# Optimization experiments

Measured on AMD Instinct MI355X. Metric: run time of the kernel, lower is better.

The kernel has to match this reference:

```python
import jax, jax.numpy as jnp
import numpy as np

N_LOCAL = 400
N_VOXEL = 200_000
N_EDGES = 1_200_000
D_LOCAL = 19
D_VOXEL = 6
NUM_CLASSES = 7
HIDDEN = 128
EPS = 1e-5  # GraphNorm eps


def _graph_norm(x, w, b, ms):
    # PyG GraphNorm with a single graph (batch=None): subtract scaled mean,
    # normalize by mean of squared centered values.
    mean = jnp.mean(x, axis=0, keepdims=True)
    out = x - ms * mean
    var = jnp.mean(out * out, axis=0, keepdims=True)
    return w * out * jax.lax.rsqrt(var + EPS) + b


def _gcn(x, src, dst, dinv, W, b, n):
    # GCNConv: symmetric-normalized aggregation with self-loops (already in src/dst)
    xw = x @ W
    msg = xw[src] * (dinv[src] * dinv[dst])[:, None]
    return jax.ops.segment_sum(msg, dst, num_segments=n) + b


def setup_inputs() -> dict:
    key = jax.random.key(0)
    ks = jax.random.split(key, 32)

    def p(k, shape, fan):
        return (jax.random.normal(k, shape, jnp.float32) / np.float32(np.sqrt(fan)))

    inp = {}
    inp["local_x"] = jax.random.normal(ks[0], (N_LOCAL, D_LOCAL), jnp.float32)
    inp["local_type"] = jax.random.randint(ks[1], (N_LOCAL,), 0, NUM_CLASSES)
    inp["voxel_x"] = jax.random.normal(ks[2], (N_VOXEL, D_VOXEL), jnp.float32)
    inp["voxel_type"] = jax.random.randint(ks[3], (N_VOXEL,), 0, NUM_CLASSES)
    inp["edge_index"] = jax.random.randint(ks[4], (2, N_EDGES), 0, N_VOXEL)
    inp["label_hard"] = jax.random.uniform(ks[5], (1, N_VOXEL, NUM_CLASSES), jnp.float32)

    din = D_LOCAL + D_VOXEL + NUM_CLASSES  # 32
    inp["We1"] = p(ks[6], (din, HIDDEN), din); inp["be1"] = jnp.zeros((HIDDEN,), jnp.float32)
    inp["We2"] = p(ks[7], (HIDDEN, HIDDEN), HIDDEN); inp["be2"] = jnp.zeros((HIDDEN,), jnp.float32)

    # encoder conv channels: 128->64->32->64->128 (REPEAT=2 down, then 2 up)
    conv_dims = [(128, 64), (64, 32), (32, 64), (64, 128)]
    for i, (a, b_) in enumerate(conv_dims):
        inp[f"Wc{i}"] = p(ks[8 + i], (a, b_), a)
        inp[f"bc{i}"] = jnp.zeros((b_,), jnp.float32)
        inp[f"gw{i}"] = jnp.ones((b_,), jnp.float32)
        inp[f"gb{i}"] = jnp.zeros((b_,), jnp.float32)
        inp[f"gm{i}"] = jnp.ones((b_,), jnp.float32)

    dec_dims = [(128, 64), (64, 32), (32, 16), (16, 1)]
    for i, (a, b_) in enumerate(dec_dims):
        inp[f"Wd{i}"] = p(ks[16 + i], (a, b_), a)
        inp[f"bd{i}"] = jnp.zeros((b_,), jnp.float32)
    return inp


def reference(local_x, local_type, voxel_x, voxel_type, edge_index, label_hard,
              We1, be1, We2, be2,
              Wc0, bc0, gw0, gb0, gm0,
              Wc1, bc1, gw1, gb1, gm1,
              Wc2, bc2, gw2, gb2, gm2,
              Wc3, bc3, gw3, gb3, gm3,
              Wd0, bd0, Wd1, bd1, Wd2, bd2, Wd3, bd3):
    n = voxel_x.shape[0]

    # --- masked type-match mean aggregation (vectorized segment mean) ---
    ones = jnp.ones((local_x.shape[0],), local_x.dtype)
    cnt = jax.ops.segment_sum(ones, local_type, num_segments=NUM_CLASSES)
    sums = jax.ops.segment_sum(local_x, local_type, num_segments=NUM_CLASSES)
    means = jnp.where(cnt[:, None] > 0, sums / jnp.maximum(cnt, 1.0)[:, None], 0.0)
    matched = means[voxel_type]  # [N_v, D_LOCAL]; zeros where type absent locally

    x = jnp.concatenate([matched, voxel_x, label_hard[0]], axis=-1)
    x = jax.nn.relu(x @ We1 + be1)
    x = jax.nn.relu(x @ We2 + be2)

    # --- GCN normalization with self-loops, computed once ---
    loop = jnp.arange(n)
    src = jnp.concatenate([edge_index[0], loop])
    dst = jnp.concatenate([edge_index[1], loop])
    deg = jax.ops.segment_sum(jnp.ones_like(dst, dtype=x.dtype), dst, num_segments=n)
    dinv = jax.lax.rsqrt(jnp.maximum(deg, 1.0))

    layers = [(Wc0, bc0, gw0, gb0, gm0), (Wc1, bc1, gw1, gb1, gm1),
              (Wc2, bc2, gw2, gb2, gm2), (Wc3, bc3, gw3, gb3, gm3)]
    for (W, b, gw, gb, gm) in layers:  # conv -> GraphNorm -> ReLU (Dropout = eval identity)
        x = _gcn(x, src, dst, dinv, W, b, n)
        x = jax.nn.relu(_graph_norm(x, gw, gb, gm))

    x = jax.nn.relu(x @ Wd0 + bd0)
    x = jax.nn.relu(x @ Wd1 + bd1)
    x = jax.nn.relu(x @ Wd2 + bd2)
    return jax.nn.sigmoid(x @ Wd3 + bd3)  # [N_v, 1]
```

## Files before the change

### kernel.cpp

```cpp
#include <hip/hip_runtime.h>
#include <hip/hip_bf16.h>
#include <cstddef>

#define THREADS 256
#define NSLOT 64

typedef unsigned short ushort_t;
typedef unsigned int uint_t;

__device__ __forceinline__ float b2f(ushort_t u) {
    union { float f; uint_t i; } v; v.i = ((uint_t)u) << 16; return v.f;
}
__device__ __forceinline__ ushort_t f2b(float f) {
    uint_t i = __float_as_uint(f);
    uint_t r = i + 0x7fffu + ((i >> 16) & 1u);
    return (ushort_t)(r >> 16);
}
__device__ __forceinline__ void unpack8(uint4 r, float* v) {
    v[0] = b2f(r.x & 0xffff); v[1] = b2f(r.x >> 16);
    v[2] = b2f(r.y & 0xffff); v[3] = b2f(r.y >> 16);
    v[4] = b2f(r.z & 0xffff); v[5] = b2f(r.z >> 16);
    v[6] = b2f(r.w & 0xffff); v[7] = b2f(r.w >> 16);
}
__device__ __forceinline__ uint4 pack8(const float* v) {
    uint4 r;
    r.x = (uint_t)f2b(v[0]) | ((uint_t)f2b(v[1]) << 16);
    r.y = (uint_t)f2b(v[2]) | ((uint_t)f2b(v[3]) << 16);
    r.z = (uint_t)f2b(v[4]) | ((uint_t)f2b(v[5]) << 16);
    r.w = (uint_t)f2b(v[6]) | ((uint_t)f2b(v[7]) << 16);
    return r;
}


__global__ __launch_bounds__(256) void local_means_kernel(const float* __restrict__ lx,
                                                          const int* __restrict__ lt,
                                                          float* __restrict__ means, int nl)
{
    __shared__ float slx[512 * 19];
    __shared__ int   slt[512];
    const int tid = threadIdx.x;
    for (int i = tid; i < nl * 19; i += 256) slx[i] = lx[i];
    for (int i = tid; i < nl; i += 256) slt[i] = lt[i];
    __syncthreads();
    if (tid >= 7 * 19) return;
    int c = tid / 19, dd = tid % 19;
    float s = 0.f; int cnt = 0;
    for (int i = 0; i < nl; ++i) {
        if (slt[i] == c) { s += slx[i * 19 + dd]; cnt++; }
    }
    means[tid] = cnt > 0 ? s / (float)cnt : 0.f;
}

__global__ void hist_kernel(const int* __restrict__ dst, int* __restrict__ degi, int E)
{
    int t = blockIdx.x * THREADS + threadIdx.x;
    if (t < E) atomicAdd(&degi[dst[t]], 1);
}


__global__ __launch_bounds__(256) void scan_part1_kernel(const int* __restrict__ degi,
                                                         int* __restrict__ blocksums, int n)
{
    const int tid = threadIdx.x;
    const int idx = blockIdx.x * 1024 + tid * 4;
    int v = 0;
    if (idx + 3 < n) {
        int4 d = *(const int4*)&degi[idx];
        v = d.x + d.y + d.z + d.w;
    } else {
        for (int i = 0; i < 4; ++i) if (idx + i < n) v += degi[idx + i];
    }
    __shared__ int s[256];
    s[tid] = v;
    __syncthreads();
    for (int off = 128; off >= 1; off >>= 1) {
        if (tid < off) s[tid] += s[tid + off];
        __syncthreads();
    }
    if (tid == 0) blocksums[blockIdx.x] = s[0];
}

__global__ __launch_bounds__(256) void scan_part2_kernel(int* __restrict__ blocksums, int nb)
{
    __shared__ int s[256];
    const int tid = threadIdx.x;
    int v = (tid < nb) ? blocksums[tid] : 0;
    s[tid] = v;
    __syncthreads();
    for (int off = 1; off < 256; off <<= 1) {
        int t = (tid >= off) ? s[tid - off] : 0;
        __syncthreads();
        s[tid] += t;
        __syncthreads();
    }
    if (tid < nb) blocksums[tid] = s[tid] - v;
}

__global__ __launch_bounds__(256) void scan_part3_kernel(const int* __restrict__ degi,
                                                         const int* __restrict__ blocksums,
                                                         int* __restrict__ rowptr,
                                                         int* __restrict__ cursor,
                                                         float* __restrict__ dinv, int n, int E)
{
    const int tid = threadIdx.x;
    const int idx = blockIdx.x * 1024 + tid * 4;
    int d0 = 0, d1 = 0, d2 = 0, d3 = 0;
    if (idx + 3 < n) {
        int4 d = *(const int4*)&degi[idx];
        d0 = d.x; d1 = d.y; d2 = d.z; d3 = d.w;
    } else {
        if (idx     < n) d0 = degi[idx];
        if (idx + 1 < n) d1 = degi[idx + 1];
        if (idx + 2 < n) d2 = degi[idx + 2];
        if (idx + 3 < n) d3 = degi[idx + 3];
    }
    const int v = d0 + d1 + d2 + d3;
    __shared__ int s[256];
    s[tid] = v;
    __syncthreads();
    for (int off = 1; off < 256; off <<= 1) {
        int t = (tid >= off) ? s[tid - off] : 0;
        __syncthreads();
        s[tid] += t;
        __syncthreads();
    }
    int run = blocksums[blockIdx.x] + s[tid] - v;
    if (idx + 3 < n) {
        int4 o;
        o.x = run; run += d0;
        o.y = run; run += d1;
        o.z = run; run += d2;
        o.w = run;
        *(int4*)&rowptr[idx] = o;
        *(int4*)&cursor[idx] = o;
        float4 dv;
        dv.x = rsqrtf((float)d0 + 1.0f);
        dv.y = rsqrtf((float)d1 + 1.0f);
        dv.z = rsqrtf((float)d2 + 1.0f);
        dv.w = rsqrtf((float)d3 + 1.0f);
        *(float4*)&dinv[idx] = dv;
    } else {
        if (idx     < n) { rowptr[idx]     = run; cursor[idx]     = run; dinv[idx]     = rsqrtf((float)d0 + 1.0f); run += d0; }
        if (idx + 1 < n) { rowptr[idx + 1] = run; cursor[idx + 1] = run; dinv[idx + 1] = rsqrtf((float)d1 + 1.0f); run += d1; }
        if (idx + 2 < n) { rowptr[idx + 2] = run; cursor[idx + 2] = run; dinv[idx + 2] = rsqrtf((float)d2 + 1.0f); run += d2; }
        if (idx + 3 < n) { rowptr[idx + 3] = run; cursor[idx + 3] = run; dinv[idx + 3] = rsqrtf((float)d3 + 1.0f); }
    }
    if (blockIdx.x == 0 && tid == 0) rowptr[n] = E;
}

__global__ void fill_kernel(const int* __restrict__ src, const int* __restrict__ dst,
                            int* __restrict__ cursor, int* __restrict__ esrc, int E)
{
    int t = blockIdx.x * THREADS + threadIdx.x;
    if (t >= E) return;
    int s = src[t], d = dst[t];
    int pos = atomicAdd(&cursor[d], 1);
    esrc[pos] = s;
}

__global__ void build_x0_kernel(const float* __restrict__ means,
                                const int* __restrict__ vt,
                                const float* __restrict__ vx,
                                const float* __restrict__ label,
                                float* __restrict__ out, int n)
{
    int tid = blockIdx.x * THREADS + threadIdx.x;
    int node = tid >> 5, c = tid & 31;
    if (node >= n) return;
    float v;
    if (c < 19)      v = means[vt[node] * 19 + c];
    else if (c < 25) v = vx[node * 6 + (c - 19)];
    else             v = label[node * 7 + (c - 25)];
    out[(size_t)node * 32 + c] = v;
}

template<int D>
__global__ void transform_kernel(const float* __restrict__ x, ushort_t* __restrict__ out,
                                 const float* __restrict__ tr, const float* __restrict__ dinv, int n)
{
    constexpr int Q = D / 8;
    int t = blockIdx.x * THREADS + threadIdx.x;
    int node = t / Q, q = t % Q;
    if (node >= n) return;
    float v[8], o[8];
    *(float4*)&v[0] = *(const float4*)&x[(size_t)node * D + q * 8];
    *(float4*)&v[4] = *(const float4*)&x[(size_t)node * D + q * 8 + 4];
    const float dd = dinv[node];
#pragma unroll
    for (int e = 0; e < 8; ++e) {
        o[e] = fmaxf(fmaf(v[e], tr[q * 8 + e], tr[D + q * 8 + e]), 0.f) * dd;
    }
    *(uint4*)&out[(size_t)node * D + q * 8] = pack8(o);
}

template<int DIN, int DOUT, int BN, int JPER, bool RELU, bool BIAS, bool TRANSFORM, bool SCALE, bool OUTBF>
__global__ __launch_bounds__(256) void mlp_kernel(
    const float* __restrict__ in, void* __restrict__ out_v,
    const float* __restrict__ W, const float* __restrict__ bias,
    const float* __restrict__ tr ,
    const float* __restrict__ rowscale, int n)
{
    constexpr int KT  = 32;
    constexpr int TJ  = DOUT / JPER;
    constexpr int TN  = 256 / TJ;
    constexpr int NPT = BN / TN;
    constexpr int JQ  = JPER / 4;
    constexpr int CS  = 4 * TJ;
    constexpr int BNP = BN + 4;

    __shared__ float Wt[KT * DOUT];
    __shared__ float xT[KT][BNP];

    const int tid   = threadIdx.x;
    const int nbase = blockIdx.x * BN;
    const int tj = tid % TJ, tn = tid / TJ;
    const int j0 = tj * 4, n0 = tn * NPT;

    float acc[NPT][JPER];
#pragma unroll
    for (int p = 0; p < NPT; ++p)
#pragma unroll
        for (int j = 0; j < JPER; ++j) acc[p][j] = 0.f;

    for (int kt = 0; kt < DIN; kt += KT) {
        __syncthreads();
        for (int i = tid * 4; i < KT * DOUT; i += THREADS * 4) {
            *(float4*)&Wt[i] = *(const float4*)&W[(size_t)kt * DOUT + i];
        }
        for (int i = tid; i < BN * (KT / 4); i += THREADS) {
            int node = i / (KT / 4);
            int kq   = i % (KT / 4);
            int g    = nbase + node;
            float4 v = make_float4(0.f, 0.f, 0.f, 0.f);
            if (g < n) {
                v = *(const float4*)&in[(size_t)g * DIN + kt + kq * 4];
                if (TRANSFORM) {
                    const float4 a = *(const float4*)&tr[kt + kq * 4];
                    const float4 c = *(const float4*)&tr[DIN + kt + kq * 4];
                    v.x = fmaxf(fmaf(v.x, a.x, c.x), 0.f);
                    v.y = fmaxf(fmaf(v.y, a.y, c.y), 0.f);
                    v.z = fmaxf(fmaf(v.z, a.z, c.z), 0.f);
                    v.w = fmaxf(fmaf(v.w, a.w, c.w), 0.f);
                }
            }
            xT[kq * 4 + 0][node] = v.x;
            xT[kq * 4 + 1][node] = v.y;
            xT[kq * 4 + 2][node] = v.z;
            xT[kq * 4 + 3][node] = v.w;
        }
        __syncthreads();
#pragma unroll 4
        for (int kk = 0; kk < KT; ++kk) {
            float wv[JPER];
#pragma unroll
            for (int q = 0; q < JQ; ++q)
                *(float4*)&wv[q * 4] = *(const float4*)&Wt[kk * DOUT + q * CS + j0];
            float xv[NPT];
#pragma unroll
            for (int q = 0; q < NPT / 4; ++q)
                *(float4*)&xv[q * 4] = *(const float4*)&xT[kk][n0 + q * 4];
#pragma unroll
            for (int p = 0; p < NPT; ++p)
#pragma unroll
                for (int j = 0; j < JPER; ++j)
                    acc[p][j] = fmaf(xv[p], wv[j], acc[p][j]);
        }
    }

    float bv[JPER];
#pragma unroll
    for (int j = 0; j < JPER; ++j) bv[j] = 0.f;
    if (BIAS) {
#pragma unroll
        for (int q = 0; q < JQ; ++q)
            *(float4*)&bv[q * 4] = *(const float4*)&bias[q * CS + j0];
    }

#pragma unroll
    for (int p = 0; p < NPT; ++p) {
        const int g = nbase + n0 + p;
        if (g >= n) continue;
        float rs = 1.f;
        if (SCALE) rs = rowscale[g];
#pragma unroll
        for (int q = 0; q < JQ; ++q) {
            float o[4];
#pragma unroll
            for (int e = 0; e < 4; ++e) {
                float x = acc[p][q * 4 + e] + bv[q * 4 + e];
                if (RELU) x = fmaxf(x, 0.f);
                if (SCALE) x *= rs;
                o[e] = x;
            }
            if (OUTBF) {
                ushort4 ob;
                ob.x = f2b(o[0]); ob.y = f2b(o[1]); ob.z = f2b(o[2]); ob.w = f2b(o[3]);
                *(ushort4*)&((ushort_t*)out_v)[(size_t)g * DOUT + q * CS + j0] = ob;
            } else {
                *(float4*)&((float*)out_v)[(size_t)g * DOUT + q * CS + j0] =
                    make_float4(o[0], o[1], o[2], o[3]);
            }
        }
    }
}

template<int D>
__global__ __launch_bounds__(256) void gather_agg_kernel(
    const ushort_t* __restrict__ y, float* __restrict__ out,
    const int* __restrict__ rowptr, const int* __restrict__ esrc,
    const float* __restrict__ dinv,
    const float* __restrict__ bias, float* __restrict__ statsP, int n)
{
    constexpr int JT  = D / 8;
    constexpr int NPB = 256 / JT;
    const int tid  = threadIdx.x;
    const int jq   = tid % JT;
    const int nsub = tid / JT;
    const int j0   = jq * 8;

    float bv[8];
#pragma unroll
    for (int e = 0; e < 8; ++e) bv[e] = bias[j0 + e];

    float s1[8], s2[8];
#pragma unroll
    for (int e = 0; e < 8; ++e) { s1[e] = 0.f; s2[e] = 0.f; }

    const int ntiles = (n + NPB - 1) / NPB;
    for (int tile = blockIdx.x; tile < ntiles; tile += gridDim.x) {
        const int node = tile * NPB + nsub;
        if (node < n) {
            const int rb = rowptr[node], re = rowptr[node + 1];
            const float dd = dinv[node];
            float acc[8];
            unpack8(*(const uint4*)&y[(size_t)node * D + j0], acc);
            int k = rb;
            for (; k + 3 < re; k += 4) {
                const int sa = esrc[k], sb = esrc[k + 1];
                const int sc = esrc[k + 2], sd = esrc[k + 3];
                const uint4 r0 = *(const uint4*)&y[(size_t)sa * D + j0];
                const uint4 r1 = *(const uint4*)&y[(size_t)sb * D + j0];
                const uint4 r2 = *(const uint4*)&y[(size_t)sc * D + j0];
                const uint4 r3 = *(const uint4*)&y[(size_t)sd * D + j0];
                float v0[8], v1[8], v2[8], v3[8];
                unpack8(r0, v0); unpack8(r1, v1); unpack8(r2, v2); unpack8(r3, v3);
#pragma unroll
                for (int e = 0; e < 8; ++e) acc[e] += (v0[e] + v1[e]) + (v2[e] + v3[e]);
            }
            for (; k < re; ++k) {
                float va[8];
                unpack8(*(const uint4*)&y[(size_t)esrc[k] * D + j0], va);
#pragma unroll
                for (int e = 0; e < 8; ++e) acc[e] += va[e];
            }
            float o[8];
#pragma unroll
            for (int e = 0; e < 8; ++e) {
                o[e] = fmaf(acc[e], dd, bv[e]);
                s1[e] += o[e];
                s2[e] = fmaf(o[e], o[e], s2[e]);
            }
            *(float4*)&out[(size_t)node * D + j0]     = make_float4(o[0], o[1], o[2], o[3]);
            *(float4*)&out[(size_t)node * D + j0 + 4] = make_float4(o[4], o[5], o[6], o[7]);
        }
    }

    __shared__ float red[256][17];
#pragma unroll
    for (int e = 0; e < 8; ++e) { red[tid][e] = s1[e]; red[tid][8 + e] = s2[e]; }
    __syncthreads();
#pragma unroll
    for (int off = NPB / 2; off >= 1; off >>= 1) {
        if (nsub < off) {
#pragma unroll
            for (int e = 0; e < 16; ++e) red[tid][e] += red[tid + off * JT][e];
        }
        __syncthreads();
    }
    if (nsub == 0) {
        float* slot = statsP + (size_t)(blockIdx.x & (NSLOT - 1)) * 256;
#pragma unroll
        for (int e = 0; e < 8; ++e) {
            atomicAdd(&slot[j0 + e],     red[tid][e]);
            atomicAdd(&slot[D + j0 + e], red[tid][8 + e]);
        }
    }
}

template<int D>
__global__ __launch_bounds__(256) void gather_pre_kernel(
    const ushort_t* __restrict__ x, float* __restrict__ out,
    const int* __restrict__ rowptr, const int* __restrict__ esrc,
    const float* __restrict__ dinv, int n)
{
    constexpr int JT  = D / 8;
    constexpr int NPB = 256 / JT;
    const int tid  = threadIdx.x;
    const int jq   = tid % JT;
    const int nsub = tid / JT;
    const int j0   = jq * 8;

    const int ntiles = (n + NPB - 1) / NPB;
    for (int tile = blockIdx.x; tile < ntiles; tile += gridDim.x) {
        const int node = tile * NPB + nsub;
        if (node < n) {
            const int rb = rowptr[node], re = rowptr[node + 1];
            const float dd = dinv[node];
            float acc[8];
            unpack8(*(const uint4*)&x[(size_t)node * D + j0], acc);
            int k = rb;
            for (; k + 3 < re; k += 4) {
                const int sa = esrc[k], sb = esrc[k + 1];
                const int sc = esrc[k + 2], sd = esrc[k + 3];
                const uint4 r0 = *(const uint4*)&x[(size_t)sa * D + j0];
                const uint4 r1 = *(const uint4*)&x[(size_t)sb * D + j0];
                const uint4 r2 = *(const uint4*)&x[(size_t)sc * D + j0];
                const uint4 r3 = *(const uint4*)&x[(size_t)sd * D + j0];
                float v0[8], v1[8], v2[8], v3[8];
                unpack8(r0, v0); unpack8(r1, v1); unpack8(r2, v2); unpack8(r3, v3);
#pragma unroll
                for (int e = 0; e < 8; ++e) acc[e] += (v0[e] + v1[e]) + (v2[e] + v3[e]);
            }
            for (; k < re; ++k) {
                float va[8];
                unpack8(*(const uint4*)&x[(size_t)esrc[k] * D + j0], va);
#pragma unroll
                for (int e = 0; e < 8; ++e) acc[e] += va[e];
            }
            float o[8];
#pragma unroll
            for (int e = 0; e < 8; ++e) o[e] = acc[e] * dd;
            *(float4*)&out[(size_t)node * D + j0]     = make_float4(o[0], o[1], o[2], o[3]);
            *(float4*)&out[(size_t)node * D + j0 + 4] = make_float4(o[4], o[5], o[6], o[7]);
        }
    }
}

template<int D>
__global__ __launch_bounds__(256) void gn_stats_kernel(const float* __restrict__ x,
                                                       float* __restrict__ statsP, int n)
{
    constexpr int JT   = D / 4;
    constexpr int NPB  = 256 / JT;
    constexpr int ITER = 32;
    const int tid  = threadIdx.x;
    const int jb   = tid % JT;
    const int rsub = tid / JT;
    const int j0   = jb * 4;
    const int base = blockIdx.x * NPB * ITER;

    float s1[4] = {0.f, 0.f, 0.f, 0.f};
    float s2[4] = {0.f, 0.f, 0.f, 0.f};

#pragma unroll 4
    for (int i = 0; i < ITER; ++i) {
        int r = base + rsub + i * NPB;
        if (r < n) {
            float4 v = *(const float4*)&x[(size_t)r * D + j0];
            s1[0] += v.x; s1[1] += v.y; s1[2] += v.z; s1[3] += v.w;
            s2[0] = fmaf(v.x, v.x, s2[0]);
            s2[1] = fmaf(v.y, v.y, s2[1]);
            s2[2] = fmaf(v.z, v.z, s2[2]);
            s2[3] = fmaf(v.w, v.w, s2[3]);
        }
    }

    __shared__ float red[256][9];
#pragma unroll
    for (int e = 0; e < 4; ++e) { red[tid][e] = s1[e]; red[tid][4 + e] = s2[e]; }
    __syncthreads();
#pragma unroll
    for (int off = NPB / 2; off >= 1; off >>= 1) {
        if (rsub < off) {
#pragma unroll
            for (int e = 0; e < 8; ++e) red[tid][e] += red[tid + off * JT][e];
        }
        __syncthreads();
    }
    if (rsub == 0) {
        float* slot = statsP + (size_t)(blockIdx.x & (NSLOT - 1)) * 256;
#pragma unroll
        for (int e = 0; e < 4; ++e) {
            atomicAdd(&slot[j0 + e],     red[tid][e]);
            atomicAdd(&slot[D + j0 + e], red[tid][4 + e]);
        }
    }
}

template<int D>
__global__ void gn_finalize_kernel(const float* __restrict__ part, float* __restrict__ ac,
                                   const float* __restrict__ gw, const float* __restrict__ gb,
                                   const float* __restrict__ gm, float inv_n)
{
    int j = threadIdx.x;
    if (j >= D) return;
    float s1 = 0.f, s2 = 0.f;
    for (int t = 0; t < NSLOT; ++t) {
        s1 += part[(size_t)t * 256 + j];
        s2 += part[(size_t)t * 256 + D + j];
    }
    float mean = s1 * inv_n;
    float ex2  = s2 * inv_n;
    float m    = gm[j];
    float var  = ex2 - (2.f * m - m * m) * mean * mean;
    float a    = gw[j] * rsqrtf(var + 1e-5f);
    float c    = gb[j] - a * m * mean;
    ac[j]     = a;
    ac[D + j] = c;
}

__global__ __launch_bounds__(256) void dec_tail_kernel(
    const float* __restrict__ in, const float* __restrict__ W1, const float* __restrict__ b1,
    const float* __restrict__ W2, const float* __restrict__ b2,
    const float* __restrict__ W3, const float* __restrict__ b3,
    float* __restrict__ out, int n)
{
    int t = blockIdx.x * THREADS + threadIdx.x;
    if (t >= n) return;

    float x[64];
#pragma unroll
    for (int q = 0; q < 16; ++q)
        *(float4*)&x[q * 4] = *(const float4*)&in[(size_t)t * 64 + q * 4];

    float h1[32];
#pragma unroll
    for (int j = 0; j < 32; ++j) h1[j] = b1[j];
#pragma unroll 8
    for (int k = 0; k < 64; ++k) {
        const float xk = x[k];
#pragma unroll
        for (int j = 0; j < 32; ++j) h1[j] = fmaf(xk, W1[k * 32 + j], h1[j]);
    }
#pragma unroll
    for (int j = 0; j < 32; ++j) h1[j] = fmaxf(h1[j], 0.f);

    float h2[16];
#pragma unroll
    for (int j = 0; j < 16; ++j) h2[j] = b2[j];
#pragma unroll 8
    for (int k = 0; k < 32; ++k) {
        const float hk = h1[k];
#pragma unroll
        for (int j = 0; j < 16; ++j) h2[j] = fmaf(hk, W2[k * 16 + j], h2[j]);
    }

    float acc = b3[0];
#pragma unroll
    for (int k = 0; k < 16; ++k) acc = fmaf(fmaxf(h2[k], 0.f), W3[k], acc);
    out[t] = 1.0f / (1.0f + expf(-acc));
}


extern "C" void kernel_launch(void* const* d_in, const int* in_sizes, int n_in,
                              void* d_out, int out_size, void* d_ws, size_t ws_size,
                              hipStream_t stream)
{
    const float* local_x    = (const float*)d_in[0];
    const int*   local_type = (const int*)d_in[1];
    const float* voxel_x    = (const float*)d_in[2];
    const int*   voxel_type = (const int*)d_in[3];
    const int*   edge_index = (const int*)d_in[4];
    const float* label      = (const float*)d_in[5];
    const float* We1 = (const float*)d_in[6],  *be1 = (const float*)d_in[7];
    const float* We2 = (const float*)d_in[8],  *be2 = (const float*)d_in[9];
    const float *Wc[4], *bc[4], *gw[4], *gb[4], *gm[4];
    for (int i = 0; i < 4; ++i) {
        Wc[i] = (const float*)d_in[10 + i * 5];
        bc[i] = (const float*)d_in[11 + i * 5];
        gw[i] = (const float*)d_in[12 + i * 5];
        gb[i] = (const float*)d_in[13 + i * 5];
        gm[i] = (const float*)d_in[14 + i * 5];
    }
    const float* Wd0 = (const float*)d_in[30], *bd0 = (const float*)d_in[31];
    const float* Wd1 = (const float*)d_in[32], *bd1 = (const float*)d_in[33];
    const float* Wd2 = (const float*)d_in[34], *bd2 = (const float*)d_in[35];
    const float* Wd3 = (const float*)d_in[36], *bd3 = (const float*)d_in[37];

    const int n  = in_sizes[2] / 6;
    const int E  = in_sizes[4] / 2;
    const int nl = in_sizes[0] / 19;
    const int* src = edge_index;
    const int* dst = edge_index + E;

    auto align256 = [](size_t x) { return (x + 255) & ~(size_t)255; };
    char* w = (char*)d_ws;
    float* ac_all = (float*)w;
    float* means  = (float*)(w + 4096);
    int* blocksums = (int*)(w + 8192);
    float* stats_part = (float*)(w + 8192 + 1024);
    size_t off = 8192 + 1024 + 4 * NSLOT * 256 * sizeof(float);
    int*   rowptr = (int*)(w + off);   off += align256((size_t)(n + 1) * 4);
    float* dinv   = (float*)(w + off); off += align256((size_t)n * 4);
    int*   esrc   = (int*)(w + off);   off += align256((size_t)E * 4);
    float* A  = (float*)(w + off);
    float* B  = A + (size_t)n * 128;
    ushort_t* Y = (ushort_t*)(B + (size_t)n * 128);
    float* A2 = A + (size_t)n * 64;
    float* B2 = B + (size_t)n * 64;
    int*   degi   = (int*)A;
    int*   cursor = (int*)A2;

    const float inv_n = 1.0f / (float)n;
    auto cdiv = [](long long a, long long b) { return (int)((a + b - 1) / b); };
    const int nb = cdiv(n, 1024);

    float* part0 = stats_part + 0 * NSLOT * 256;
    float* part1 = stats_part + 1 * NSLOT * 256;
    float* part2 = stats_part + 2 * NSLOT * 256;
    float* part3 = stats_part + 3 * NSLOT * 256;
    float* ac0 = ac_all + 0, *ac1 = ac_all + 256, *ac2 = ac_all + 512, *ac3 = ac_all + 768;

    hipMemsetAsync(stats_part, 0, 4 * NSLOT * 256 * sizeof(float), stream);
    hipMemsetAsync(degi, 0, (size_t)n * sizeof(int), stream);

    local_means_kernel<<<1, 256, 0, stream>>>(local_x, local_type, means, nl);
    hist_kernel<<<cdiv(E, 256), 256, 0, stream>>>(dst, degi, E);
    scan_part1_kernel<<<nb, 256, 0, stream>>>(degi, blocksums, n);
    scan_part2_kernel<<<1, 256, 0, stream>>>(blocksums, nb);
    scan_part3_kernel<<<nb, 256, 0, stream>>>(degi, blocksums, rowptr, cursor, dinv, n, E);
    fill_kernel<<<cdiv(E, 256), 256, 0, stream>>>(src, dst, cursor, esrc, E);
    build_x0_kernel<<<cdiv((long long)n * 32, 256), 256, 0, stream>>>(means, voxel_type, voxel_x, label, B, n);

    const int gagg = 2048;

    mlp_kernel<32, 128, 128, 8, true, true, false, false, false><<<cdiv(n, 128), 256, 0, stream>>>(B, A, We1, be1, nullptr, nullptr, n);
    mlp_kernel<128, 128, 128, 8, true, true, false, false, false><<<cdiv(n, 128), 256, 0, stream>>>(A, B, We2, be2, nullptr, nullptr, n);

    mlp_kernel<128, 64, 256, 8, false, false, false, true, true><<<cdiv(n, 256), 256, 0, stream>>>(B, Y, Wc[0], nullptr, nullptr, dinv, n);
    gather_agg_kernel<64><<<gagg, 256, 0, stream>>>(Y, A2, rowptr, esrc, dinv, bc[0], part0, n);
    gn_finalize_kernel<64><<<1, 64, 0, stream>>>(part0, ac0, gw[0], gb[0], gm[0], inv_n);

    mlp_kernel<64, 32, 256, 4, false, false, true, true, true><<<cdiv(n, 256), 256, 0, stream>>>(A2, Y, Wc[1], nullptr, ac0, dinv, n);
    gather_agg_kernel<32><<<gagg, 256, 0, stream>>>(Y, B2, rowptr, esrc, dinv, bc[1], part1, n);
    gn_finalize_kernel<32><<<1, 32, 0, stream>>>(part1, ac1, gw[1], gb[1], gm[1], inv_n);

    transform_kernel<32><<<cdiv((long long)n * 4, 256), 256, 0, stream>>>(B2, Y, ac1, dinv, n);
    gather_pre_kernel<32><<<gagg, 256, 0, stream>>>(Y, A, rowptr, esrc, dinv, n);
    mlp_kernel<32, 64, 256, 8, false, true, false, false, false><<<cdiv(n, 256), 256, 0, stream>>>(A, A2, Wc[2], bc[2], nullptr, nullptr, n);
    gn_stats_kernel<64><<<cdiv(n, 512), 256, 0, stream>>>(A2, part2, n);
    gn_finalize_kernel<64><<<1, 64, 0, stream>>>(part2, ac2, gw[2], gb[2], gm[2], inv_n);

    transform_kernel<64><<<cdiv((long long)n * 8, 256), 256, 0, stream>>>(A2, Y, ac2, dinv, n);
    gather_pre_kernel<64><<<gagg, 256, 0, stream>>>(Y, B, rowptr, esrc, dinv, n);
    mlp_kernel<64, 128, 128, 8, false, true, false, false, false><<<cdiv(n, 128), 256, 0, stream>>>(B, A, Wc[3], bc[3], nullptr, nullptr, n);
    gn_stats_kernel<128><<<cdiv(n, 256), 256, 0, stream>>>(A, part3, n);
    gn_finalize_kernel<128><<<1, 128, 0, stream>>>(part3, ac3, gw[3], gb[3], gm[3], inv_n);

    mlp_kernel<128, 64, 256, 8, true, true, true, false, false><<<cdiv(n, 256), 256, 0, stream>>>(A, B, Wd0, bd0, ac3, nullptr, n);
    dec_tail_kernel<<<cdiv(n, 256), 256, 0, stream>>>(B, Wd1, bd1, Wd2, bd2, Wd3, bd3, (float*)d_out, n);
}
```

Measured before the change: 812.1 us.

## Use bf16 MFMA for large MLP layers and switch gather buffers to fp32

Adds an MFMA-based matmul kernel that converts activations and weights to bf16 in shared memory and uses 16x16x32 bf16 matrix instructions for the 128-wide layers. It replaces the FMA tiled kernel for the second encoder layer, the first conv, the last conv and the first decoder layer. At the same time the intermediate gather buffers go from bf16 to fp32, which removes pack/unpack work but doubles bytes moved in the edge gathers. The MFMA epilogue writes scalar per-column stores, which may coalesce less well.

```diff
diff --git a/kernel.cpp b/kernel.cpp
--- a/kernel.cpp
+++ b/kernel.cpp
@@ -7,28 +7,13 @@
 
 typedef unsigned short ushort_t;
 typedef unsigned int uint_t;
-
-__device__ __forceinline__ float b2f(ushort_t u) {
-    union { float f; uint_t i; } v; v.i = ((uint_t)u) << 16; return v.f;
-}
+typedef __attribute__((ext_vector_type(8))) short bf16x8;
+typedef __attribute__((ext_vector_type(4))) float f32x4;
+
 __device__ __forceinline__ ushort_t f2b(float f) {
     uint_t i = __float_as_uint(f);
     uint_t r = i + 0x7fffu + ((i >> 16) & 1u);
     return (ushort_t)(r >> 16);
-}
-__device__ __forceinline__ void unpack8(uint4 r, float* v) {
-    v[0] = b2f(r.x & 0xffff); v[1] = b2f(r.x >> 16);
-    v[2] = b2f(r.y & 0xffff); v[3] = b2f(r.y >> 16);
-    v[4] = b2f(r.z & 0xffff); v[5] = b2f(r.z >> 16);
-    v[6] = b2f(r.w & 0xffff); v[7] = b2f(r.w >> 16);
-}
-__device__ __forceinline__ uint4 pack8(const float* v) {
-    uint4 r;
-    r.x = (uint_t)f2b(v[0]) | ((uint_t)f2b(v[1]) << 16);
-    r.y = (uint_t)f2b(v[2]) | ((uint_t)f2b(v[3]) << 16);
-    r.z = (uint_t)f2b(v[4]) | ((uint_t)f2b(v[5]) << 16);
-    r.w = (uint_t)f2b(v[6]) | ((uint_t)f2b(v[7]) << 16);
-    return r;
 }
 
 
@@ -56,7 +41,6 @@
     int t = blockIdx.x * THREADS + threadIdx.x;
     if (t < E) atomicAdd(&degi[dst[t]], 1);
 }
-
 
 __global__ __launch_bounds__(256) void scan_part1_kernel(const int* __restrict__ degi,
                                                          int* __restrict__ blocksums, int n)
@@ -175,30 +159,30 @@
 }
 
 template<int D>
-__global__ void transform_kernel(const float* __restrict__ x, ushort_t* __restrict__ out,
+__global__ void transform_kernel(const float* __restrict__ x, float* __restrict__ out,
                                  const float* __restrict__ tr, const float* __restrict__ dinv, int n)
 {
-    constexpr int Q = D / 8;
+    constexpr int Q = D / 4;
     int t = blockIdx.x * THREADS + threadIdx.x;
     int node = t / Q, q = t % Q;
     if (node >= n) return;
-    float v[8], o[8];
-    *(float4*)&v[0] = *(const float4*)&x[(size_t)node * D + q * 8];
-    *(float4*)&v[4] = *(const float4*)&x[(size_t)node * D + q * 8 + 4];
+    float4 v = *(const float4*)&x[(size_t)node * D + q * 4];
+    const float4 a = *(const float4*)&tr[q * 4];
+    const float4 c = *(const float4*)&tr[D + q * 4];
     const float dd = dinv[node];
-#pragma unroll
-    for (int e = 0; e < 8; ++e) {
-        o[e] = fmaxf(fmaf(v[e], tr[q * 8 + e], tr[D + q * 8 + e]), 0.f) * dd;
-    }
-    *(uint4*)&out[(size_t)node * D + q * 8] = pack8(o);
-}
-
-template<int DIN, int DOUT, int BN, int JPER, bool RELU, bool BIAS, bool TRANSFORM, bool SCALE, bool OUTBF>
+    float4 o;
+    o.x = fmaxf(fmaf(v.x, a.x, c.x), 0.f) * dd;
+    o.y = fmaxf(fmaf(v.y, a.y, c.y), 0.f) * dd;
+    o.z = fmaxf(fmaf(v.z, a.z, c.z), 0.f) * dd;
+    o.w = fmaxf(fmaf(v.w, a.w, c.w), 0.f) * dd;
+    *(float4*)&out[(size_t)node * D + q * 4] = o;
+}
+
+template<int DIN, int DOUT, int BN, int JPER, bool RELU, bool BIAS, bool TRANSFORM, bool SCALE>
 __global__ __launch_bounds__(256) void mlp_kernel(
-    const float* __restrict__ in, void* __restrict__ out_v,
+    const float* __restrict__ in, float* __restrict__ out,
     const float* __restrict__ W, const float* __restrict__ bias,
-    const float* __restrict__ tr ,
-    const float* __restrict__ rowscale, int n)
+    const float* __restrict__ tr, const float* __restrict__ rowscale, int n)
 {
     constexpr int KT  = 32;
     constexpr int TJ  = DOUT / JPER;
@@ -284,21 +268,126 @@
         if (SCALE) rs = rowscale[g];
 #pragma unroll
         for (int q = 0; q < JQ; ++q) {
-            float o[4];
-#pragma unroll
-            for (int e = 0; e < 4; ++e) {
-                float x = acc[p][q * 4 + e] + bv[q * 4 + e];
-                if (RELU) x = fmaxf(x, 0.f);
-                if (SCALE) x *= rs;
-                o[e] = x;
-            }
-            if (OUTBF) {
-                ushort4 ob;
-                ob.x = f2b(o[0]); ob.y = f2b(o[1]); ob.z = f2b(o[2]); ob.w = f2b(o[3]);
-                *(ushort4*)&((ushort_t*)out_v)[(size_t)g * DOUT + q * CS + j0] = ob;
-            } else {
-                *(float4*)&((float*)out_v)[(size_t)g * DOUT + q * CS + j0] =
-                    make_float4(o[0], o[1], o[2], o[3]);
+            float4 o;
+            o.x = acc[p][q * 4 + 0] + bv[q * 4 + 0];
+            o.y = acc[p][q * 4 + 1] + bv[q * 4 + 1];
+            o.z = acc[p][q * 4 + 2] + bv[q * 4 + 2];
+            o.w = acc[p][q * 4 + 3] + bv[q * 4 + 3];
+            if (RELU) {
+                o.x = fmaxf(o.x, 0.f); o.y = fmaxf(o.y, 0.f);
+                o.z = fmaxf(o.z, 0.f); o.w = fmaxf(o.w, 0.f);
+            }
+            if (SCALE) { o.x *= rs; o.y *= rs; o.z *= rs; o.w *= rs; }
+            *(float4*)&out[(size_t)g * DOUT + q * CS + j0] = o;
+        }
+    }
+}
+
+template<int DIN, int DOUT, bool RELU, bool BIAS, bool TRANSFORM, bool SCALE>
+__global__ __launch_bounds__(256) void mfma_mlp_kernel(
+    const float* __restrict__ in, float* __restrict__ out,
+    const float* __restrict__ W, const float* __restrict__ bias,
+    const float* __restrict__ tr, const float* __restrict__ rowscale, int n)
+{
+    constexpr int BN  = 128;
+    constexpr int KT  = 32;
+    constexpr int NT  = DIN / KT;
+    constexpr int LDK = 40;
+    constexpr int WM  = 2, WN = 2;
+    constexpr int MW  = BN / WM;
+    constexpr int NW  = DOUT / WN;
+    constexpr int MR  = MW / 16;
+    constexpr int NR  = NW / 16;
+
+    __shared__ ushort_t xA[BN * LDK];
+    __shared__ ushort_t wB[DOUT * LDK];
+
+    const int tid   = threadIdx.x;
+    const int wid   = tid >> 6;
+    const int lane  = tid & 63;
+    const int wm    = wid >> 1, wn = wid & 1;
+    const int nbase = blockIdx.x * BN;
+    const int l16   = lane & 15;
+    const int lk8   = (lane >> 4) * 8;
+
+    f32x4 acc[MR][NR];
+#pragma unroll
+    for (int mi = 0; mi < MR; ++mi)
+#pragma unroll
+        for (int ni = 0; ni < NR; ++ni)
+#pragma unroll
+            for (int j = 0; j < 4; ++j) acc[mi][ni][j] = 0.f;
+
+    for (int t = 0; t < NT; ++t) {
+        const int kt = t * KT;
+        __syncthreads();
+        for (int i = tid; i < BN * (KT / 4); i += 256) {
+            const int row = i / (KT / 4);
+            const int kq  = (i % (KT / 4)) * 4;
+            const int g   = nbase + row;
+            float4 v = make_float4(0.f, 0.f, 0.f, 0.f);
+            if (g < n) {
+                v = *(const float4*)&in[(size_t)g * DIN + kt + kq];
+                if (TRANSFORM) {
+                    const float4 a = *(const float4*)&tr[kt + kq];
+                    const float4 c = *(const float4*)&tr[DIN + kt + kq];
+                    v.x = fmaxf(fmaf(v.x, a.x, c.x), 0.f);
+                    v.y = fmaxf(fmaf(v.y, a.y, c.y), 0.f);
+                    v.z = fmaxf(fmaf(v.z, a.z, c.z), 0.f);
+                    v.w = fmaxf(fmaf(v.w, a.w, c.w), 0.f);
+                }
+            }
+            ushort4 b;
+            b.x = f2b(v.x); b.y = f2b(v.y); b.z = f2b(v.z); b.w = f2b(v.w);
+            *(ushort4*)&xA[row * LDK + kq] = b;
+        }
+        for (int i = tid; i < (KT * DOUT) / 4; i += 256) {
+            const int k = (i * 4) / DOUT;
+            const int c = (i * 4) % DOUT;
+            float4 v = *(const float4*)&W[(size_t)(kt + k) * DOUT + c];
+            wB[(c + 0) * LDK + k] = f2b(v.x);
+            wB[(c + 1) * LDK + k] = f2b(v.y);
+            wB[(c + 2) * LDK + k] = f2b(v.z);
+            wB[(c + 3) * LDK + k] = f2b(v.w);
+        }
+        __syncthreads();
+
+        bf16x8 af[MR], bf[NR];
+#pragma unroll
+        for (int mi = 0; mi < MR; ++mi)
+            af[mi] = *(const bf16x8*)&xA[(wm * MW + mi * 16 + l16) * LDK + lk8];
+#pragma unroll
+        for (int ni = 0; ni < NR; ++ni)
+            bf[ni] = *(const bf16x8*)&wB[(wn * NW + ni * 16 + l16) * LDK + lk8];
+#pragma unroll
+        for (int mi = 0; mi < MR; ++mi)
+#pragma unroll
+            for (int ni = 0; ni < NR; ++ni)
+                acc[mi][ni] = __builtin_amdgcn_mfma_f32_16x16x32_bf16(
+                    af[mi], bf[ni], acc[mi][ni], 0, 0, 0);
+    }
+
+    float bv[NR];
+#pragma unroll
+    for (int ni = 0; ni < NR; ++ni)
+        bv[ni] = BIAS ? bias[wn * NW + ni * 16 + l16] : 0.f;
+
+#pragma unroll
+    for (int mi = 0; mi < MR; ++mi) {
+#pragma unroll
+        for (int j = 0; j < 4; ++j) {
+            const int r = wm * MW + mi * 16 + (lane >> 4) * 4 + j;
+            const int g = nbase + r;
+            if (g >= n) continue;
+            float rs = 1.f;
+            if (SCALE) rs = rowscale[g];
+#pragma unroll
+            for (int ni = 0; ni < NR; ++ni) {
+                const int col = wn * NW + ni * 16 + l16;
+                float v = acc[mi][ni][j] + bv[ni];
+                if (RELU) v = fmaxf(v, 0.f);
+                if (SCALE) v *= rs;
+                out[(size_t)g * DOUT + col] = v;
             }
         }
     }
@@ -306,7 +395,7 @@
 
 template<int D>
 __global__ __launch_bounds__(256) void gather_agg_kernel(
-    const ushort_t* __restrict__ y, float* __restrict__ out,
+    const float* __restrict__ y, float* __restrict__ out,
     const int* __restrict__ rowptr, const int* __restrict__ esrc,
     const float* __restrict__ dinv,
     const float* __restrict__ bias, float* __restrict__ statsP, int n)
@@ -333,25 +422,26 @@
             const int rb = rowptr[node], re = rowptr[node + 1];
             const float dd = dinv[node];
             float acc[8];
-            unpack8(*(const uint4*)&y[(size_t)node * D + j0], acc);
+            *(float4*)&acc[0] = *(const float4*)&y[(size_t)node * D + j0];
+            *(float4*)&acc[4] = *(const float4*)&y[(size_t)node * D + j0 + 4];
             int k = rb;
-            for (; k + 3 < re; k += 4) {
+            for (; k + 1 < re; k += 2) {
                 const int sa = esrc[k], sb = esrc[k + 1];
-                const int sc = esrc[k + 2], sd = esrc[k + 3];
-                const uint4 r0 = *(const uint4*)&y[(size_t)sa * D + j0];
-                const uint4 r1 = *(const uint4*)&y[(size_t)sb * D + j0];
-                const uint4 r2 = *(const uint4*)&y[(size_t)sc * D + j0];
-                const uint4 r3 = *(const uint4*)&y[(size_t)sd * D + j0];
-                float v0[8], v1[8], v2[8], v3[8];
-                unpack8(r0, v0); unpack8(r1, v1); unpack8(r2, v2); unpack8(r3, v3);
-#pragma unroll
-                for (int e = 0; e < 8; ++e) acc[e] += (v0[e] + v1[e]) + (v2[e] + v3[e]);
-            }
-            for (; k < re; ++k) {
-                float va[8];
-                unpack8(*(const uint4*)&y[(size_t)esrc[k] * D + j0], va);
-#pragma unroll
-                for (int e = 0; e < 8; ++e) acc[e] += va[e];
+                float4 a0 = *(const float4*)&y[(size_t)sa * D + j0];
+                float4 a1 = *(const float4*)&y[(size_t)sa * D + j0 + 4];
+                float4 b0 = *(const float4*)&y[(size_t)sb * D + j0];
+                float4 b1 = *(const float4*)&y[(size_t)sb * D + j0 + 4];
+                acc[0] += a0.x + b0.x; acc[1] += a0.y + b0.y;
+                acc[2] += a0.z + b0.z; acc[3] += a0.w + b0.w;
+                acc[4] += a1.x + b1.x; acc[5] += a1.y + b1.y;
+                acc[6] += a1.z + b1.z; acc[7] += a1.w + b1.w;
+            }
+            if (k < re) {
+                const int sa = esrc[k];
+                float4 a0 = *(const float4*)&y[(size_t)sa * D + j0];
+                float4 a1 = *(const float4*)&y[(size_t)sa * D + j0 + 4];
+                acc[0] += a0.x; acc[1] += a0.y; acc[2] += a0.z; acc[3] += a0.w;
+                acc[4] += a1.x; acc[5] += a1.y; acc[6] += a1.z; acc[7] += a1.w;
             }
             float o[8];
 #pragma unroll
@@ -389,7 +479,7 @@
 
 template<int D>
 __global__ __launch_bounds__(256) void gather_pre_kernel(
-    const ushort_t* __restrict__ x, float* __restrict__ out,
+    const float* __restrict__ x, float* __restrict__ out,
     const int* __restrict__ rowptr, const int* __restrict__ esrc,
     const float* __restrict__ dinv, int n)
 {
@@ -407,31 +497,31 @@
             const int rb = rowptr[node], re = rowptr[node + 1];
             const float dd = dinv[node];
             float acc[8];
-            unpack8(*(const uint4*)&x[(size_t)node * D + j0], acc);
+            *(float4*)&acc[0] = *(const float4*)&x[(size_t)node * D + j0];
+            *(float4*)&acc[4] = *(const float4*)&x[(size_t)node * D + j0 + 4];
             int k = rb;
-            for (; k + 3 < re; k += 4) {
+            for (; k + 1 < re; k += 2) {
                 const int sa = esrc[k], sb = esrc[k + 1];
-                const int sc = esrc[k + 2], sd = esrc[k + 3];
-                const uint4 r0 = *(const uint4*)&x[(size_t)sa * D + j0];
-                const uint4 r1 = *(const uint4*)&x[(size_t)sb * D + j0];
-                const uint4 r2 = *(const uint4*)&x[(size_t)sc * D + j0];
-                const uint4 r3 = *(const uint4*)&x[(size_t)sd * D + j0];
-                float v0[8], v1[8], v2[8], v3[8];
-                unpack8(r0, v0); unpack8(r1, v1); unpack8(r2, v2); unpack8(r3, v3);
-#pragma unroll
-                for (int e = 0; e < 8; ++e) acc[e] += (v0[e] + v1[e]) + (v2[e] + v3[e]);
-            }
-            for (; k < re; ++k) {
-                float va[8];
-                unpack8(*(const uint4*)&x[(size_t)esrc[k] * D + j0], va);
-#pragma unroll
-                for (int e = 0; e < 8; ++e) acc[e] += va[e];
-            }
-            float o[8];
-#pragma unroll
-            for (int e = 0; e < 8; ++e) o[e] = acc[e] * dd;
-            *(float4*)&out[(size_t)node * D + j0]     = make_float4(o[0], o[1], o[2], o[3]);
-            *(float4*)&out[(size_t)node * D + j0 + 4] = make_float4(o[4], o[5], o[6], o[7]);
+                float4 a0 = *(const float4*)&x[(size_t)sa * D + j0];
+                float4 a1 = *(const float4*)&x[(size_t)sa * D + j0 + 4];
+                float4 b0 = *(const float4*)&x[(size_t)sb * D + j0];
+                float4 b1 = *(const float4*)&x[(size_t)sb * D + j0 + 4];
+                acc[0] += a0.x + b0.x; acc[1] += a0.y + b0.y;
+                acc[2] += a0.z + b0.z; acc[3] += a0.w + b0.w;
+                acc[4] += a1.x + b1.x; acc[5] += a1.y + b1.y;
+                acc[6] += a1.z + b1.z; acc[7] += a1.w + b1.w;
+            }
+            if (k < re) {
+                const int sa = esrc[k];
+                float4 a0 = *(const float4*)&x[(size_t)sa * D + j0];
+                float4 a1 = *(const float4*)&x[(size_t)sa * D + j0 + 4];
+                acc[0] += a0.x; acc[1] += a0.y; acc[2] += a0.z; acc[3] += a0.w;
+                acc[4] += a1.x; acc[5] += a1.y; acc[6] += a1.z; acc[7] += a1.w;
+            }
+            float4 o0 = make_float4(acc[0] * dd, acc[1] * dd, acc[2] * dd, acc[3] * dd);
+            float4 o1 = make_float4(acc[4] * dd, acc[5] * dd, acc[6] * dd, acc[7] * dd);
+            *(float4*)&out[(size_t)node * D + j0]     = o0;
+            *(float4*)&out[(size_t)node * D + j0 + 4] = o1;
         }
     }
 }
@@ -593,13 +683,14 @@
     int*   rowptr = (int*)(w + off);   off += align256((size_t)(n + 1) * 4);
     float* dinv   = (float*)(w + off); off += align256((size_t)n * 4);
     int*   esrc   = (int*)(w + off);   off += align256((size_t)E * 4);
-    float* A  = (float*)(w + off);
-    float* B  = A + (size_t)n * 128;
-    ushort_t* Y = (ushort_t*)(B + (size_t)n * 128);
-    float* A2 = A + (size_t)n * 64;
-    float* B2 = B + (size_t)n * 64;
+    float* A    = (float*)(w + off);
+    float* B    = A + (size_t)n * 128;
+    float* A_lo = A;
+    float* A_hi = A + (size_t)n * 64;
+    float* B_lo = B;
+    float* B_hi = B + (size_t)n * 64;
     int*   degi   = (int*)A;
-    int*   cursor = (int*)A2;
+    int*   cursor = (int*)A_hi;
 
     const float inv_n = 1.0f / (float)n;
     auto cdiv = [](long long a, long long b) { return (int)((a + b - 1) / b); };
@@ -620,33 +711,34 @@
     scan_part2_kernel<<<1, 256, 0, stream>>>(blocksums, nb);
     scan_part3_kernel<<<nb, 256, 0, stream>>>(degi, blocksums, rowptr, cursor, dinv, n, E);
     fill_kernel<<<cdiv(E, 256), 256, 0, stream>>>(src, dst, cursor, esrc, E);
-    build_x0_kernel<<<cdiv((long long)n * 32, 256), 256, 0, stream>>>(means, voxel_type, voxel_x, label, B, n);
-
-    const int gagg = 2048;
-
-    mlp_kernel<32, 128, 128, 8, true, true, false, false, false><<<cdiv(n, 128), 256, 0, stream>>>(B, A, We1, be1, nullptr, nullptr, n);
-    mlp_kernel<128, 128, 128, 8, true, true, false, false, false><<<cdiv(n, 128), 256, 0, stream>>>(A, B, We2, be2, nullptr, nullptr, n);
-
-    mlp_kernel<128, 64, 256, 8, false, false, false, true, true><<<cdiv(n, 256), 256, 0, stream>>>(B, Y, Wc[0], nullptr, nullptr, dinv, n);
-    gather_agg_kernel<64><<<gagg, 256, 0, stream>>>(Y, A2, rowptr, esrc, dinv, bc[0], part0, n);
+    build_x0_kernel<<<cdiv((long long)n * 32, 256), 256, 0, stream>>>(means, voxel_type, voxel_x, label, B_lo, n);
+
+    const int gagg  = 2048;
+    const int gmfma = cdiv(n, 128);
+
+    mlp_kernel<32, 128, 128, 8, true, true, false, false><<<cdiv(n, 128), 256, 0, stream>>>(B_lo, A, We1, be1, nullptr, nullptr, n);
+    mfma_mlp_kernel<128, 128, true, true, false, false><<<gmfma, 256, 0, stream>>>(A, B, We2, be2, nullptr, nullptr, n);
+
+    mfma_mlp_kernel<128, 64, false, false, false, true><<<gmfma, 256, 0, stream>>>(B, A_lo, Wc[0], nullptr, nullptr, dinv, n);
+    gather_agg_kernel<64><<<gagg, 256, 0, stream>>>(A_lo, A_hi, rowptr, esrc, dinv, bc[0], part0, n);
     gn_finalize_kernel<64><<<1, 64, 0, stream>>>(part0, ac0, gw[0], gb[0], gm[0], inv_n);
 
-    mlp_kernel<64, 32, 256, 4, false, false, true, true, true><<<cdiv(n, 256), 256, 0, stream>>>(A2, Y, Wc[1], nullptr, ac0, dinv, n);
-    gather_agg_kernel<32><<<gagg, 256, 0, stream>>>(Y, B2, rowptr, esrc, dinv, bc[1], part1, n);
+    mlp_kernel<64, 32, 256, 4, false, false, true, true><<<cdiv(n, 256), 256, 0, stream>>>(A_hi, B_lo, Wc[1], nullptr, ac0, dinv, n);
+    gather_agg_kernel<32><<<gagg, 256, 0, stream>>>(B_lo, B_hi, rowptr, esrc, dinv, bc[1], part1, n);
     gn_finalize_kernel<32><<<1, 32, 0, stream>>>(part1, ac1, gw[1], gb[1], gm[1], inv_n);
 
-    transform_kernel<32><<<cdiv((long long)n * 4, 256), 256, 0, stream>>>(B2, Y, ac1, dinv, n);
-    gather_pre_kernel<32><<<gagg, 256, 0, stream>>>(Y, A, rowptr, esrc, dinv, n);
-    mlp_kernel<32, 64, 256, 8, false, true, false, false, false><<<cdiv(n, 256), 256, 0, stream>>>(A, A2, Wc[2], bc[2], nullptr, nullptr, n);
-    gn_stats_kernel<64><<<cdiv(n, 512), 256, 0, stream>>>(A2, part2, n);
+    transform_kernel<32><<<cdiv((long long)n * 8, 256), 256, 0, stream>>>(B_hi, B_lo, ac1, dinv, n);
+    gather_pre_kernel<32><<<gagg, 256, 0, stream>>>(B_lo, A_lo, rowptr, esrc, dinv, n);
+    mlp_kernel<32, 64, 256, 8, false, true, false, false><<<cdiv(n, 256), 256, 0, stream>>>(A_lo, B_hi, Wc[2], bc[2], nullptr, nullptr, n);
+    gn_stats_kernel<64><<<cdiv(n, 512), 256, 0, stream>>>(B_hi, part2, n);
     gn_finalize_kernel<64><<<1, 64, 0, stream>>>(part2, ac2, gw[2], gb[2], gm[2], inv_n);
 
-    transform_kernel<64><<<cdiv((long long)n * 8, 256), 256, 0, stream>>>(A2, Y, ac2, dinv, n);
-    gather_pre_kernel<64><<<gagg, 256, 0, stream>>>(Y, B, rowptr, esrc, dinv, n);
-    mlp_kernel<64, 128, 128, 8, false, true, false, false, false><<<cdiv(n, 128), 256, 0, stream>>>(B, A, Wc[3], bc[3], nullptr, nullptr, n);
+    transform_kernel<64><<<cdiv((long long)n * 16, 256), 256, 0, stream>>>(B_hi, A_lo, ac2, dinv, n);
+    gather_pre_kernel<64><<<gagg, 256, 0, stream>>>(A_lo, B_lo, rowptr, esrc, dinv, n);
+    mfma_mlp_kernel<64, 128, false, true, false, false><<<gmfma, 256, 0, stream>>>(B_lo, A, Wc[3], bc[3], nullptr, nullptr, n);
     gn_stats_kernel<128><<<cdiv(n, 256), 256, 0, stream>>>(A, part3, n);
     gn_finalize_kernel<128><<<1, 128, 0, stream>>>(part3, ac3, gw[3], gb[3], gm[3], inv_n);
 
-    mlp_kernel<128, 64, 256, 8, true, true, true, false, false><<<cdiv(n, 256), 256, 0, stream>>>(A, B, Wd0, bd0, ac3, nullptr, n);
-    dec_tail_kernel<<<cdiv(n, 256), 256, 0, stream>>>(B, Wd1, bd1, Wd2, bd2, Wd3, bd3, (float*)d_out, n);
-}
+    mfma_mlp_kernel<128, 64, true, true, true, false><<<gmfma, 256, 0, stream>>>(A, B_lo, Wd0, bd0, ac3, nullptr, n);
+    dec_tail_kernel<<<cdiv(n, 256), 256, 0, stream>>>(B_lo, Wd1, bd1, Wd2, bd2, Wd3, bd3, (float*)d_out, n);
+}
```

After: 732.6 us. 1.11x faster.
